# Performance work log

Measured on AMD Instinct MI355X. Metric: run time of the kernel, lower is better.

## Reference

```python
import jax, jax.numpy as jnp
import numpy as np

B, S, D_IN = 16, 512, 768
HID, OUT = 64, 12
NEG = 1e12


def setup_inputs() -> dict:
    key = jax.random.key(0)
    k1, k2, k3 = jax.random.split(key, 3)
    x = jax.random.normal(k1, (B, S, D_IN), dtype=jnp.float32)
    mask = jnp.ones((B, S), dtype=jnp.float32)
    W = jax.random.normal(k2, (D_IN, HID * OUT * 2), dtype=jnp.float32) * 0.02
    b = jax.random.normal(k3, (HID * OUT * 2,), dtype=jnp.float32) * 0.02
    return {"x": x, "mask": mask, "W": W, "b": b}


def reference(x, mask, W, b):
    Bb, Ss, _ = x.shape
    h, out = HID, OUT
    # QKV-style projection, split into `out` heads of 2h each
    proj = (x @ W + b).reshape(Bb, Ss, out, 2 * h)  # [b, s, out, 2h]
    qw, kw = proj[..., :h], proj[..., h:]           # [b, s, out, h]

    # Sinusoidal position embedding (merge='zero'): interleaved sin/cos
    pos_ids = jnp.arange(Ss, dtype=x.dtype)
    inv_freq = jnp.power(10000.0, -2.0 * jnp.arange(h // 2, dtype=x.dtype) / h)
    ang = pos_ids[:, None] * inv_freq               # [s, h/2]
    sin, cos = jnp.sin(ang), jnp.cos(ang)
    # torch: pos[..., None, 1::2].repeat(1,1,1,2) -> TILED (not interleaved)
    cos_pos = jnp.concatenate([cos, cos], axis=-1)[None, :, None, :]  # [1, s, 1, h]
    sin_pos = jnp.concatenate([sin, sin], axis=-1)[None, :, None, :]

    def rope(w):
        # stack([-w_odd, w_even], -1).reshape -> interleaved rotation partner
        w2 = jnp.stack([-w[..., 1::2], w[..., ::2]], axis=-1).reshape(w.shape)
        return w * cos_pos + w2 * sin_pos

    qw = rope(qw)
    kw = rope(kw)

    logits = jnp.einsum('bmhd,bnhd->bhmn', qw, kw)  # [b, out, s, s]

    pad = mask[:, None, None, :]                    # broadcast over [b, out, s, s]
    logits = logits * pad - (1.0 - pad) * NEG

    tril = jnp.tril(jnp.ones((Ss, Ss), dtype=logits.dtype), -1)
    logits = logits - tril * NEG

    return logits / (h ** 0.5)
```

## Files before the change

### kernel.cpp

```cpp
#include <hip/hip_runtime.h>
#include <stdint.h>

#define DIN   768
#define NPROJ 1536
#define SEQ   512
#define NHEAD 12
#define NBATCH 16
#define NEGV  1000000000000.0f

typedef short bf16x8 __attribute__((ext_vector_type(8)));
typedef float f32x4  __attribute__((ext_vector_type(4)));

__device__ __forceinline__ unsigned short f2bf(float f) {
    union { float f; unsigned int u; } v; v.f = f;
    return (unsigned short)((v.u + 0x7FFFu + ((v.u >> 16) & 1u)) >> 16);
}
__device__ __forceinline__ float bf2f(unsigned short u) {
    union { unsigned int u; float f; } v; v.u = ((unsigned int)u) << 16;
    return v.f;
}

__global__ __launch_bounds__(256) void k_trig(float* __restrict__ trig) {
    int gi = blockIdx.x * 256 + threadIdx.x;
    int ss = gi >> 5, j = gi & 31;
    const float C = 0.41524101186092034f;
    float cs, sn;
    sincosf((float)ss * exp2f(-(float)j * C), &sn, &cs);
    trig[2 * gi]     = cs;
    trig[2 * gi + 1] = sn;
}

__global__ __launch_bounds__(256) void k_xcast(const float* __restrict__ X,
                                               unsigned short* __restrict__ Xb) {
    int i = (blockIdx.x * 256 + threadIdx.x) * 4;
    float4 v = *(const float4*)&X[i];
    short4 s;
    s.x = (short)f2bf(v.x); s.y = (short)f2bf(v.y);
    s.z = (short)f2bf(v.z); s.w = (short)f2bf(v.w);
    *(short4*)&Xb[i] = s;
}

__global__ __launch_bounds__(256) void k_wt(const float* __restrict__ W,
                                            unsigned short* __restrict__ Wt) {
    __shared__ unsigned short T[64][72];
    const int n0 = blockIdx.x * 64, k0 = blockIdx.y * 64;
    const int tid = threadIdx.x;
#pragma unroll
    for (int it = 0; it < 4; it++) {
        int c = tid + it * 256;
        int kl = c >> 4, nl = (c & 15) * 4;
        float4 v = *(const float4*)&W[(size_t)(k0 + kl) * NPROJ + n0 + nl];
        T[nl + 0][kl] = f2bf(v.x);
        T[nl + 1][kl] = f2bf(v.y);
        T[nl + 2][kl] = f2bf(v.z);
        T[nl + 3][kl] = f2bf(v.w);
    }
    __syncthreads();
#pragma unroll
    for (int it = 0; it < 2; it++) {
        int c = tid + it * 256;
        int nl = c >> 3, kb = (c & 7) * 8;
        *(int4*)&Wt[(size_t)(n0 + nl) * DIN + k0 + kb] = *(int4*)&T[nl][kb];
    }
}

template <bool PRE>
__global__ __launch_bounds__(256) void k_gemm(const float* __restrict__ X,
                                              const unsigned short* __restrict__ Xb,
                                              const unsigned short* __restrict__ Wt,
                                              const float* __restrict__ bias,
                                              const float* __restrict__ trig,
                                              unsigned short* __restrict__ P) {
    __shared__ unsigned short smem[2 * 128 * 72];
    unsigned short* sA = smem;
    unsigned short* sB = smem + 128 * 72;
    const int tid = threadIdx.x;
    const int m0 = blockIdx.y * 128, n0 = blockIdx.x * 128;
    const int lane = tid & 63, w = tid >> 6;
    const int q = lane >> 4, r = lane & 15;
    const int wm = w >> 1, wn = w & 1;
    f32x4 acc[4][4];
#pragma unroll
    for (int i = 0; i < 4; i++)
#pragma unroll
        for (int j = 0; j < 4; j++) acc[i][j] = (f32x4){0.f, 0.f, 0.f, 0.f};

    for (int k0 = 0; k0 < DIN; k0 += 64) {
        __syncthreads();
        if (PRE) {
#pragma unroll
            for (int it = 0; it < 4; it++) {
                int c = tid + it * 256;
                int row = c >> 3, col = (c & 7) * 8;
                *(int4*)&sA[row * 72 + col] =
                    *(const int4*)&Xb[(size_t)(m0 + row) * DIN + k0 + col];
            }
        } else {
#pragma unroll
            for (int it = 0; it < 8; it++) {
                int c = tid + it * 256;
                int row = c >> 4, col = (c & 15) * 4;
                float4 v = *(const float4*)&X[(size_t)(m0 + row) * DIN + k0 + col];
                short4 sv;
                sv.x = (short)f2bf(v.x); sv.y = (short)f2bf(v.y);
                sv.z = (short)f2bf(v.z); sv.w = (short)f2bf(v.w);
                *(short4*)&sA[row * 72 + col] = sv;
            }
        }
#pragma unroll
        for (int it = 0; it < 4; it++) {
            int c = tid + it * 256;
            int row = c >> 3, col = (c & 7) * 8;
            *(int4*)&sB[row * 72 + col] =
                *(const int4*)&Wt[(size_t)(n0 + row) * DIN + k0 + col];
        }
        __syncthreads();
#pragma unroll
        for (int kk = 0; kk < 64; kk += 32) {
            bf16x8 af[4], bfr[4];
#pragma unroll
            for (int t = 0; t < 4; t++)
                af[t] = *(const bf16x8*)&sA[(wm * 64 + t * 16 + r) * 72 + kk + q * 8];
#pragma unroll
            for (int t = 0; t < 4; t++)
                bfr[t] = *(const bf16x8*)&sB[(wn * 64 + t * 16 + r) * 72 + kk + q * 8];
#pragma unroll
            for (int tm = 0; tm < 4; tm++)
#pragma unroll
                for (int tn = 0; tn < 4; tn++)
                    acc[tm][tn] = __builtin_amdgcn_mfma_f32_16x16x32_bf16(
                        af[tm], bfr[tn], acc[tm][tn], 0, 0, 0);
        }
    }
    float bb[4];
#pragma unroll
    for (int tn = 0; tn < 4; tn++) bb[tn] = bias[n0 + wn * 64 + tn * 16 + r];
    __syncthreads();
    unsigned short* sT = smem;
#pragma unroll
    for (int tm = 0; tm < 4; tm++) {
        int rowb = wm * 64 + tm * 16 + q * 4;
#pragma unroll
        for (int tn = 0; tn < 4; tn++) {
            int col = wn * 64 + tn * 16 + r;
#pragma unroll
            for (int i = 0; i < 4; i++)
                sT[(rowb + i) * 136 + col] = f2bf(acc[tm][tn][i] + bb[tn]);
        }
    }
    __syncthreads();
#pragma unroll
    for (int it = 0; it < 8; it++) {
        int c = tid + it * 256;
        int row = c >> 4, colb = (c & 15) * 8;
        int m = m0 + row;
        int s = m & (SEQ - 1);
        int base = colb & 31;
        union { int4 v; unsigned short u[8]; } pk;
        pk.v = *(int4*)&sT[row * 136 + colb];
        float wv[8];
#pragma unroll
        for (int j = 0; j < 8; j++) wv[j] = bf2f(pk.u[j]);
        const float* tp = &trig[2 * (s * 32 + base)];
#pragma unroll
        for (int p = 0; p < 4; p++) {
            float4 tt = *(const float4*)&tp[4 * p];
            float oe = wv[2 * p] * tt.x - wv[2 * p + 1] * tt.y;
            float oo = wv[2 * p + 1] * tt.z + wv[2 * p] * tt.w;
            pk.u[2 * p]     = f2bf(oe);
            pk.u[2 * p + 1] = f2bf(oo);
        }
        *(int4*)&P[(size_t)m * NPROJ + n0 + colb] = pk.v;
    }
}

__global__ __launch_bounds__(256) void k_attn(const unsigned short* __restrict__ P,
                                              const float* __restrict__ mask,
                                              float* __restrict__ out) {
    __shared__ unsigned short smem[2 * 128 * 72];
    unsigned short* sQ = smem;
    unsigned short* sK = smem + 128 * 72;
    const int tid = threadIdx.x;
    const int b = blockIdx.z, h = blockIdx.y;
    const int mt = blockIdx.x >> 2, nt = blockIdx.x & 3;
    const size_t obase = ((size_t)((b * NHEAD + h) * SEQ)) * SEQ;

    if (nt < mt) {
#pragma unroll
        for (int it = 0; it < 16; it++) {
            int c = tid + it * 256;
            int rl = c >> 5, cb = (c & 31) * 4;
            int m = mt * 128 + rl, n = nt * 128 + cb;
            f32x4 mk = *(const f32x4*)&mask[b * SEQ + n];
            f32x4 o;
#pragma unroll
            for (int j = 0; j < 4; j++)
                o[j] = (-(1.f - mk[j]) * NEGV - NEGV) * 0.125f;
            __builtin_nontemporal_store(o, (f32x4*)&out[obase + (size_t)m * SEQ + n]);
        }
        return;
    }

#pragma unroll
    for (int it = 0; it < 4; it++) {
        int c = tid + it * 256;
        int row = c >> 3, col = (c & 7) * 8;
        size_t gq = (size_t)(b * SEQ + mt * 128 + row) * NPROJ + h * 128 + col;
        *(int4*)&sQ[row * 72 + col] = *(const int4*)&P[gq];
        size_t gk = (size_t)(b * SEQ + nt * 128 + row) * NPROJ + h * 128 + 64 + col;
        *(int4*)&sK[row * 72 + col] = *(const int4*)&P[gk];
    }
    __syncthreads();
    const int lane = tid & 63, w = tid >> 6;
    const int q = lane >> 4, r = lane & 15;
    const int wm = w >> 1, wn = w & 1;
    f32x4 acc[4][4];
#pragma unroll
    for (int i = 0; i < 4; i++)
#pragma unroll
        for (int j = 0; j < 4; j++) acc[i][j] = (f32x4){0.f, 0.f, 0.f, 0.f};
#pragma unroll
    for (int kk = 0; kk < 64; kk += 32) {
        bf16x8 af[4], bfr[4];
#pragma unroll
        for (int t = 0; t < 4; t++)
            af[t] = *(const bf16x8*)&sQ[(wm * 64 + t * 16 + r) * 72 + kk + q * 8];
#pragma unroll
        for (int t = 0; t < 4; t++)
            bfr[t] = *(const bf16x8*)&sK[(wn * 64 + t * 16 + r) * 72 + kk + q * 8];
#pragma unroll
        for (int tm = 0; tm < 4; tm++)
#pragma unroll
            for (int tn = 0; tn < 4; tn++)
                acc[tm][tn] = __builtin_amdgcn_mfma_f32_16x16x32_bf16(
                    af[tm], bfr[tn], acc[tm][tn], 0, 0, 0);
    }
    float* sbuf = (float*)smem;
    const int rowb = wm * 16 + q * 4;
#pragma unroll
    for (int tm = 0; tm < 4; tm++) {
        __syncthreads();
#pragma unroll
        for (int tn = 0; tn < 4; tn++) {
            int col = wn * 64 + tn * 16 + r;
#pragma unroll
            for (int i = 0; i < 4; i++)
                sbuf[(rowb + i) * 132 + col] = acc[tm][tn][i];
        }
        __syncthreads();
#pragma unroll
        for (int it = 0; it < 4; it++) {
            int c = tid + it * 256;
            int rl = c >> 5, cb = (c & 31) * 4;
            f32x4 v = *(f32x4*)&sbuf[rl * 132 + cb];
            int m = mt * 128 + (rl >> 4) * 64 + tm * 16 + (rl & 15);
            int n = nt * 128 + cb;
            f32x4 mk = *(const f32x4*)&mask[b * SEQ + n];
            f32x4 o;
#pragma unroll
            for (int j = 0; j < 4; j++)
                o[j] = (v[j] * mk[j] - (1.f - mk[j]) * NEGV
                        - ((n + j) < m ? NEGV : 0.f)) * 0.125f;
            __builtin_nontemporal_store(o, (f32x4*)&out[obase + (size_t)m * SEQ + n]);
        }
    }
}

extern "C" void kernel_launch(void* const* d_in, const int* in_sizes, int n_in,
                              void* d_out, int out_size, void* d_ws, size_t ws_size,
                              hipStream_t stream) {
    const float* x    = (const float*)d_in[0];
    const float* mask = (const float*)d_in[1];
    const float* W    = (const float*)d_in[2];
    const float* bias = (const float*)d_in[3];
    float* out = (float*)d_out;

    const size_t wtN = (size_t)NPROJ * DIN;
    const size_t pN  = (size_t)NBATCH * SEQ * NPROJ;
    const size_t xN  = (size_t)NBATCH * SEQ * DIN;
    const size_t trigN = (size_t)SEQ * 32 * 2;
    unsigned short* Wt = (unsigned short*)d_ws;
    unsigned short* P  = Wt + wtN;
    float* trig        = (float*)(P + pN);
    unsigned short* Xb = (unsigned short*)(trig + trigN);
    const bool pre = ws_size >= (wtN + pN) * sizeof(unsigned short)
                               + trigN * sizeof(float)
                               + xN * sizeof(unsigned short);

    k_trig<<<SEQ * 32 / 256, 256, 0, stream>>>(trig);
    k_wt<<<dim3(NPROJ / 64, DIN / 64), 256, 0, stream>>>(W, Wt);
    if (pre) {
        k_xcast<<<(int)(xN / (256 * 4)), 256, 0, stream>>>(x, Xb);
        k_gemm<true><<<dim3(NPROJ / 128, (NBATCH * SEQ) / 128), 256, 0, stream>>>(
            x, Xb, Wt, bias, trig, P);
    } else {
        k_gemm<false><<<dim3(NPROJ / 128, (NBATCH * SEQ) / 128), 256, 0, stream>>>(
            x, nullptr, Wt, bias, trig, P);
    }
    k_attn<<<dim3(16, NHEAD, NBATCH), 256, 0, stream>>>(P, mask, out);
}
```

Before: 277.0 us.

## Fuse prep kernels, use direct global-to-LDS loads with swizzle, loop attn over column tiles

Merges the trig, weight-transpose and x-cast kernels into one launch to cut launch overhead. The GEMM and attention staging now use global_load_lds with an XOR-swizzled unpadded layout instead of register round-trips into padded shared memory. The attention kernel now runs one block per row tile and loops over four column tiles, reusing Q fragments held in registers. That removes repeated Q loads but gives fewer blocks and more serial work per block, and diagonal-heavy rows get uneven work.

```diff
diff --git a/kernel.cpp b/kernel.cpp
--- a/kernel.cpp
+++ b/kernel.cpp
@@ -10,6 +10,7 @@
 
 typedef short bf16x8 __attribute__((ext_vector_type(8)));
 typedef float f32x4  __attribute__((ext_vector_type(4)));
+typedef unsigned short u16x8 __attribute__((ext_vector_type(8)));
 
 __device__ __forceinline__ unsigned short f2bf(float f) {
     union { float f; unsigned int u; } v; v.f = f;
@@ -20,48 +21,72 @@
     return v.f;
 }
 
-__global__ __launch_bounds__(256) void k_trig(float* __restrict__ trig) {
-    int gi = blockIdx.x * 256 + threadIdx.x;
-    int ss = gi >> 5, j = gi & 31;
-    const float C = 0.41524101186092034f;
-    float cs, sn;
-    sincosf((float)ss * exp2f(-(float)j * C), &sn, &cs);
-    trig[2 * gi]     = cs;
-    trig[2 * gi + 1] = sn;
-}
-
-__global__ __launch_bounds__(256) void k_xcast(const float* __restrict__ X,
-                                               unsigned short* __restrict__ Xb) {
-    int i = (blockIdx.x * 256 + threadIdx.x) * 4;
+__device__ __forceinline__ void gl_lds16(const unsigned short* g, unsigned short* l) {
+    __builtin_amdgcn_global_load_lds(
+        (const __attribute__((address_space(1))) unsigned int*)(uintptr_t)g,
+        (__attribute__((address_space(3))) unsigned int*)(uintptr_t)l,
+        16, 0, 0);
+}
+
+__device__ __forceinline__ void stage128x64(const unsigned short* __restrict__ g,
+                                            int gstride, unsigned short* lds,
+                                            int w, int lane) {
+#pragma unroll
+    for (int t = 0; t < 4; t++) {
+        int lr = w * 32 + t * 8 + (lane >> 3);
+        int c16 = (lane & 7) ^ (lr & 7);
+        gl_lds16(g + (size_t)lr * gstride + c16 * 8,
+                 lds + (w * 32 + t * 8) * 64);
+    }
+}
+__device__ __forceinline__ int swz(int row, int cg) {
+    return row * 64 + ((cg ^ (row & 7)) << 3);
+}
+
+__global__ __launch_bounds__(256) void k_prep(const float* __restrict__ X,
+                                              unsigned short* __restrict__ Xb,
+                                              const float* __restrict__ W,
+                                              unsigned short* __restrict__ Wt,
+                                              float* __restrict__ trig) {
+    __shared__ unsigned short T[64][72];
+    const int bid = blockIdx.x, tid = threadIdx.x;
+    if (bid < 288) {
+        int n0 = (bid % 24) * 64, k0 = (bid / 24) * 64;
+#pragma unroll
+        for (int it = 0; it < 4; it++) {
+            int c = tid + it * 256;
+            int kl = c >> 4, nl = (c & 15) * 4;
+            float4 v = *(const float4*)&W[(size_t)(k0 + kl) * NPROJ + n0 + nl];
+            T[nl + 0][kl] = f2bf(v.x);
+            T[nl + 1][kl] = f2bf(v.y);
+            T[nl + 2][kl] = f2bf(v.z);
+            T[nl + 3][kl] = f2bf(v.w);
+        }
+        __syncthreads();
+#pragma unroll
+        for (int it = 0; it < 2; it++) {
+            int c = tid + it * 256;
+            int nl = c >> 3, kb = (c & 7) * 8;
+            *(int4*)&Wt[(size_t)(n0 + nl) * DIN + k0 + kb] = *(int4*)&T[nl][kb];
+        }
+        return;
+    }
+    if (bid < 352) {
+        int gi = (bid - 288) * 256 + tid;
+        int ss = gi >> 5, j = gi & 31;
+        const float C = 0.41524101186092034f;
+        float cs, sn;
+        sincosf((float)ss * exp2f(-(float)j * C), &sn, &cs);
+        trig[2 * gi]     = cs;
+        trig[2 * gi + 1] = sn;
+        return;
+    }
+    int i = ((bid - 352) * 256 + tid) * 4;
     float4 v = *(const float4*)&X[i];
     short4 s;
     s.x = (short)f2bf(v.x); s.y = (short)f2bf(v.y);
     s.z = (short)f2bf(v.z); s.w = (short)f2bf(v.w);
     *(short4*)&Xb[i] = s;
-}
-
-__global__ __launch_bounds__(256) void k_wt(const float* __restrict__ W,
-                                            unsigned short* __restrict__ Wt) {
-    __shared__ unsigned short T[64][72];
-    const int n0 = blockIdx.x * 64, k0 = blockIdx.y * 64;
-    const int tid = threadIdx.x;
-#pragma unroll
-    for (int it = 0; it < 4; it++) {
-        int c = tid + it * 256;
-        int kl = c >> 4, nl = (c & 15) * 4;
-        float4 v = *(const float4*)&W[(size_t)(k0 + kl) * NPROJ + n0 + nl];
-        T[nl + 0][kl] = f2bf(v.x);
-        T[nl + 1][kl] = f2bf(v.y);
-        T[nl + 2][kl] = f2bf(v.z);
-        T[nl + 3][kl] = f2bf(v.w);
-    }
-    __syncthreads();
-#pragma unroll
-    for (int it = 0; it < 2; it++) {
-        int c = tid + it * 256;
-        int nl = c >> 3, kb = (c & 7) * 8;
-        *(int4*)&Wt[(size_t)(n0 + nl) * DIN + k0 + kb] = *(int4*)&T[nl][kb];
-    }
 }
 
 template <bool PRE>
@@ -71,9 +96,9 @@
                                               const float* __restrict__ bias,
                                               const float* __restrict__ trig,
                                               unsigned short* __restrict__ P) {
-    __shared__ unsigned short smem[2 * 128 * 72];
+    __shared__ unsigned short smem[17408];
     unsigned short* sA = smem;
-    unsigned short* sB = smem + 128 * 72;
+    unsigned short* sB = smem + 8192;
     const int tid = threadIdx.x;
     const int m0 = blockIdx.y * 128, n0 = blockIdx.x * 128;
     const int lane = tid & 63, w = tid >> 6;
@@ -85,45 +110,41 @@
 #pragma unroll
         for (int j = 0; j < 4; j++) acc[i][j] = (f32x4){0.f, 0.f, 0.f, 0.f};
 
+    const unsigned short* Ag = Xb + (size_t)m0 * DIN;
+    const unsigned short* Bg = Wt + (size_t)n0 * DIN;
+
     for (int k0 = 0; k0 < DIN; k0 += 64) {
         __syncthreads();
         if (PRE) {
+            stage128x64(Ag + k0, DIN, sA, w, lane);
+        } else {
 #pragma unroll
             for (int it = 0; it < 4; it++) {
                 int c = tid + it * 256;
-                int row = c >> 3, col = (c & 7) * 8;
-                *(int4*)&sA[row * 72 + col] =
-                    *(const int4*)&Xb[(size_t)(m0 + row) * DIN + k0 + col];
-            }
-        } else {
-#pragma unroll
-            for (int it = 0; it < 8; it++) {
-                int c = tid + it * 256;
-                int row = c >> 4, col = (c & 15) * 4;
-                float4 v = *(const float4*)&X[(size_t)(m0 + row) * DIN + k0 + col];
-                short4 sv;
-                sv.x = (short)f2bf(v.x); sv.y = (short)f2bf(v.y);
-                sv.z = (short)f2bf(v.z); sv.w = (short)f2bf(v.w);
-                *(short4*)&sA[row * 72 + col] = sv;
-            }
-        }
-#pragma unroll
-        for (int it = 0; it < 4; it++) {
-            int c = tid + it * 256;
-            int row = c >> 3, col = (c & 7) * 8;
-            *(int4*)&sB[row * 72 + col] =
-                *(const int4*)&Wt[(size_t)(n0 + row) * DIN + k0 + col];
-        }
+                int row = c >> 3, c16 = c & 7;
+                const float* xp = &X[(size_t)(m0 + row) * DIN + k0 + c16 * 8];
+                float4 v0 = *(const float4*)xp;
+                float4 v1 = *(const float4*)(xp + 4);
+                u16x8 sv;
+                sv[0] = f2bf(v0.x); sv[1] = f2bf(v0.y);
+                sv[2] = f2bf(v0.z); sv[3] = f2bf(v0.w);
+                sv[4] = f2bf(v1.x); sv[5] = f2bf(v1.y);
+                sv[6] = f2bf(v1.z); sv[7] = f2bf(v1.w);
+                *(u16x8*)&sA[swz(row, c16)] = sv;
+            }
+        }
+        stage128x64(Bg + k0, DIN, sB, w, lane);
         __syncthreads();
 #pragma unroll
         for (int kk = 0; kk < 64; kk += 32) {
+            const int cg = (kk >> 3) + q;
             bf16x8 af[4], bfr[4];
 #pragma unroll
             for (int t = 0; t < 4; t++)
-                af[t] = *(const bf16x8*)&sA[(wm * 64 + t * 16 + r) * 72 + kk + q * 8];
+                af[t] = *(const bf16x8*)&sA[swz(wm * 64 + t * 16 + r, cg)];
 #pragma unroll
             for (int t = 0; t < 4; t++)
-                bfr[t] = *(const bf16x8*)&sB[(wn * 64 + t * 16 + r) * 72 + kk + q * 8];
+                bfr[t] = *(const bf16x8*)&sB[swz(wn * 64 + t * 16 + r, cg)];
 #pragma unroll
             for (int tm = 0; tm < 4; tm++)
 #pragma unroll
@@ -177,91 +198,98 @@
 __global__ __launch_bounds__(256) void k_attn(const unsigned short* __restrict__ P,
                                               const float* __restrict__ mask,
                                               float* __restrict__ out) {
-    __shared__ unsigned short smem[2 * 128 * 72];
-    unsigned short* sQ = smem;
-    unsigned short* sK = smem + 128 * 72;
+    __shared__ unsigned short sQ[8192], sK[8192];
+    __shared__ float sbuf[32 * 132];
     const int tid = threadIdx.x;
-    const int b = blockIdx.z, h = blockIdx.y;
-    const int mt = blockIdx.x >> 2, nt = blockIdx.x & 3;
-    const size_t obase = ((size_t)((b * NHEAD + h) * SEQ)) * SEQ;
-
-    if (nt < mt) {
-#pragma unroll
-        for (int it = 0; it < 16; it++) {
-            int c = tid + it * 256;
-            int rl = c >> 5, cb = (c & 31) * 4;
-            int m = mt * 128 + rl, n = nt * 128 + cb;
-            f32x4 mk = *(const f32x4*)&mask[b * SEQ + n];
-            f32x4 o;
-#pragma unroll
-            for (int j = 0; j < 4; j++)
-                o[j] = (-(1.f - mk[j]) * NEGV - NEGV) * 0.125f;
-            __builtin_nontemporal_store(o, (f32x4*)&out[obase + (size_t)m * SEQ + n]);
-        }
-        return;
-    }
-
-#pragma unroll
-    for (int it = 0; it < 4; it++) {
-        int c = tid + it * 256;
-        int row = c >> 3, col = (c & 7) * 8;
-        size_t gq = (size_t)(b * SEQ + mt * 128 + row) * NPROJ + h * 128 + col;
-        *(int4*)&sQ[row * 72 + col] = *(const int4*)&P[gq];
-        size_t gk = (size_t)(b * SEQ + nt * 128 + row) * NPROJ + h * 128 + 64 + col;
-        *(int4*)&sK[row * 72 + col] = *(const int4*)&P[gk];
-    }
-    __syncthreads();
+    const int b = blockIdx.z, h = blockIdx.y, mt = blockIdx.x;
     const int lane = tid & 63, w = tid >> 6;
     const int q = lane >> 4, r = lane & 15;
     const int wm = w >> 1, wn = w & 1;
-    f32x4 acc[4][4];
-#pragma unroll
-    for (int i = 0; i < 4; i++)
-#pragma unroll
-        for (int j = 0; j < 4; j++) acc[i][j] = (f32x4){0.f, 0.f, 0.f, 0.f};
-#pragma unroll
-    for (int kk = 0; kk < 64; kk += 32) {
-        bf16x8 af[4], bfr[4];
-#pragma unroll
-        for (int t = 0; t < 4; t++)
-            af[t] = *(const bf16x8*)&sQ[(wm * 64 + t * 16 + r) * 72 + kk + q * 8];
-#pragma unroll
-        for (int t = 0; t < 4; t++)
-            bfr[t] = *(const bf16x8*)&sK[(wn * 64 + t * 16 + r) * 72 + kk + q * 8];
-#pragma unroll
-        for (int tm = 0; tm < 4; tm++)
-#pragma unroll
-            for (int tn = 0; tn < 4; tn++)
-                acc[tm][tn] = __builtin_amdgcn_mfma_f32_16x16x32_bf16(
-                    af[tm], bfr[tn], acc[tm][tn], 0, 0, 0);
-    }
-    float* sbuf = (float*)smem;
-    const int rowb = wm * 16 + q * 4;
-#pragma unroll
-    for (int tm = 0; tm < 4; tm++) {
-        __syncthreads();
-#pragma unroll
-        for (int tn = 0; tn < 4; tn++) {
-            int col = wn * 64 + tn * 16 + r;
-#pragma unroll
-            for (int i = 0; i < 4; i++)
-                sbuf[(rowb + i) * 132 + col] = acc[tm][tn][i];
-        }
-        __syncthreads();
-#pragma unroll
-        for (int it = 0; it < 4; it++) {
-            int c = tid + it * 256;
-            int rl = c >> 5, cb = (c & 31) * 4;
-            f32x4 v = *(f32x4*)&sbuf[rl * 132 + cb];
-            int m = mt * 128 + (rl >> 4) * 64 + tm * 16 + (rl & 15);
-            int n = nt * 128 + cb;
-            f32x4 mk = *(const f32x4*)&mask[b * SEQ + n];
-            f32x4 o;
-#pragma unroll
-            for (int j = 0; j < 4; j++)
-                o[j] = (v[j] * mk[j] - (1.f - mk[j]) * NEGV
-                        - ((n + j) < m ? NEGV : 0.f)) * 0.125f;
-            __builtin_nontemporal_store(o, (f32x4*)&out[obase + (size_t)m * SEQ + n]);
+    const size_t obase = ((size_t)((b * NHEAD + h) * SEQ)) * SEQ;
+
+    const unsigned short* Qg = P + (size_t)(b * SEQ + mt * 128) * NPROJ + h * 128;
+    stage128x64(Qg, NPROJ, sQ, w, lane);
+
+    bf16x8 aq[2][4];
+    bool qload = false;
+    for (int nt = 0; nt < 4; nt++) {
+        const int ncol0 = nt * 128;
+        if (nt < mt) {
+#pragma unroll
+            for (int it = 0; it < 16; it++) {
+                int c = tid + it * 256;
+                int rl = c >> 5, cb = (c & 31) * 4;
+                int m = mt * 128 + rl, n = ncol0 + cb;
+                f32x4 mk = *(const f32x4*)&mask[b * SEQ + n];
+                f32x4 o;
+#pragma unroll
+                for (int j = 0; j < 4; j++)
+                    o[j] = (-(1.f - mk[j]) * NEGV - NEGV) * 0.125f;
+                __builtin_nontemporal_store(o, (f32x4*)&out[obase + (size_t)m * SEQ + n]);
+            }
+            continue;
+        }
+        __syncthreads();
+        const unsigned short* Kg =
+            P + (size_t)(b * SEQ + nt * 128) * NPROJ + h * 128 + 64;
+        stage128x64(Kg, NPROJ, sK, w, lane);
+        __syncthreads();
+        if (!qload) {
+            qload = true;
+#pragma unroll
+            for (int x2 = 0; x2 < 2; x2++) {
+                int cg = x2 * 4 + q;
+#pragma unroll
+                for (int t = 0; t < 4; t++)
+                    aq[x2][t] = *(const bf16x8*)&sQ[swz(wm * 64 + t * 16 + r, cg)];
+            }
+        }
+        f32x4 acc[4][4];
+#pragma unroll
+        for (int i = 0; i < 4; i++)
+#pragma unroll
+            for (int j = 0; j < 4; j++) acc[i][j] = (f32x4){0.f, 0.f, 0.f, 0.f};
+#pragma unroll
+        for (int x2 = 0; x2 < 2; x2++) {
+            int cg = x2 * 4 + q;
+            bf16x8 bfr[4];
+#pragma unroll
+            for (int t = 0; t < 4; t++)
+                bfr[t] = *(const bf16x8*)&sK[swz(wn * 64 + t * 16 + r, cg)];
+#pragma unroll
+            for (int tm = 0; tm < 4; tm++)
+#pragma unroll
+                for (int tn = 0; tn < 4; tn++)
+                    acc[tm][tn] = __builtin_amdgcn_mfma_f32_16x16x32_bf16(
+                        aq[x2][tm], bfr[tn], acc[tm][tn], 0, 0, 0);
+        }
+        const int rowb = wm * 16 + q * 4;
+#pragma unroll
+        for (int tm = 0; tm < 4; tm++) {
+            __syncthreads();
+#pragma unroll
+            for (int tn = 0; tn < 4; tn++) {
+                int col = wn * 64 + tn * 16 + r;
+#pragma unroll
+                for (int i = 0; i < 4; i++)
+                    sbuf[(rowb + i) * 132 + col] = acc[tm][tn][i];
+            }
+            __syncthreads();
+#pragma unroll
+            for (int it = 0; it < 4; it++) {
+                int c = tid + it * 256;
+                int rl = c >> 5, cb = (c & 31) * 4;
+                f32x4 v = *(f32x4*)&sbuf[rl * 132 + cb];
+                int m = mt * 128 + (rl >> 4) * 64 + tm * 16 + (rl & 15);
+                int n = ncol0 + cb;
+                f32x4 mk = *(const f32x4*)&mask[b * SEQ + n];
+                f32x4 o;
+#pragma unroll
+                for (int j = 0; j < 4; j++)
+                    o[j] = (v[j] * mk[j] - (1.f - mk[j]) * NEGV
+                            - ((n + j) < m ? NEGV : 0.f)) * 0.125f;
+                __builtin_nontemporal_store(o, (f32x4*)&out[obase + (size_t)m * SEQ + n]);
+            }
         }
     }
 }
@@ -275,27 +303,25 @@
     const float* bias = (const float*)d_in[3];
     float* out = (float*)d_out;
 
-    const size_t wtN = (size_t)NPROJ * DIN;
-    const size_t pN  = (size_t)NBATCH * SEQ * NPROJ;
-    const size_t xN  = (size_t)NBATCH * SEQ * DIN;
+    const size_t wtN   = (size_t)NPROJ * DIN;
+    const size_t pN    = (size_t)NBATCH * SEQ * NPROJ;
+    const size_t xN    = (size_t)NBATCH * SEQ * DIN;
     const size_t trigN = (size_t)SEQ * 32 * 2;
     unsigned short* Wt = (unsigned short*)d_ws;
     unsigned short* P  = Wt + wtN;
     float* trig        = (float*)(P + pN);
     unsigned short* Xb = (unsigned short*)(trig + trigN);
-    const bool pre = ws_size >= (wtN + pN) * sizeof(unsigned short)
-                               + trigN * sizeof(float)
-                               + xN * sizeof(unsigned short);
-
-    k_trig<<<SEQ * 32 / 256, 256, 0, stream>>>(trig);
-    k_wt<<<dim3(NPROJ / 64, DIN / 64), 256, 0, stream>>>(W, Wt);
+    const bool pre = ws_size >= (wtN + pN + xN) * sizeof(unsigned short)
+                               + trigN * sizeof(float);
+
+    const int xblocks = (int)(xN / 1024);
+    k_prep<<<pre ? (352 + xblocks) : 352, 256, 0, stream>>>(x, Xb, W, Wt, trig);
     if (pre) {
-        k_xcast<<<(int)(xN / (256 * 4)), 256, 0, stream>>>(x, Xb);
         k_gemm<true><<<dim3(NPROJ / 128, (NBATCH * SEQ) / 128), 256, 0, stream>>>(
             x, Xb, Wt, bias, trig, P);
     } else {
         k_gemm<false><<<dim3(NPROJ / 128, (NBATCH * SEQ) / 128), 256, 0, stream>>>(
             x, nullptr, Wt, bias, trig, P);
     }
-    k_attn<<<dim3(16, NHEAD, NBATCH), 256, 0, stream>>>(P, mask, out);
-}
+    k_attn<<<dim3(4, NHEAD, NBATCH), 256, 0, stream>>>(P, mask, out);
+}
```

Measured after the change: 273.8 us. Within noise of the previous version (-1.1%).
